# Kernel optimization log

Hardware: AMD Instinct MI355X
Metric: run time of the kernel (lower is better)

The kernel has to match this reference:

```python
import jax, jax.numpy as jnp
import numpy as np

SIZE = 48          # sinkhorn_canvas_size
EPS = 0.01         # entropy regularization
ITERS = 5          # sinkhorn iterations
CHANNEL = 0        # fixed channel (original picks a random one of 3)


def _build_cost_matrix(size):
    y, x = jnp.meshgrid(jnp.arange(size), jnp.arange(size), indexing='ij')
    pixels = jnp.stack((y.flatten(), x.flatten()), axis=1).astype(jnp.float32) / size  # [N,2]
    diff = pixels[:, None, :] - pixels[None, :, :]  # [N,N,2]
    return jnp.sum(diff * diff, axis=-1)            # [N,N]


def setup_inputs() -> dict:
    key = jax.random.key(0)
    k1, k2 = jax.random.split(key)
    B = 32
    img_pred = jax.random.uniform(k1, (B, 3, SIZE, SIZE), dtype=jnp.float32)
    img_target = jax.random.uniform(k2, (B, 3, SIZE, SIZE), dtype=jnp.float32)
    cost_matrix = _build_cost_matrix(SIZE)
    return {"img_pred": img_pred, "img_target": img_target, "cost_matrix": cost_matrix}


def reference(img_pred, img_target, cost_matrix):
    B = img_pred.shape[0]
    # fixed channel, flatten spatial dims -> [B, N]
    p = img_pred[:, CHANNEL].reshape(B, -1) + 1e-9
    t = img_target[:, CHANNEL].reshape(B, -1) + 1e-9
    mass_source = p / jnp.sum(p, axis=-1, keepdims=True)
    mass_target = t / jnp.sum(t, axis=-1, keepdims=True)
    log_u = jnp.log(mass_source)
    log_v = jnp.log(mass_target)
    u = jnp.zeros_like(mass_source)
    v = jnp.zeros_like(mass_target)

    def M(u, v):
        # modified cost for log-domain updates: [B, N, N]
        return (-cost_matrix[None, :, :] + u[:, :, None] + v[:, None, :]) / EPS

    def lse(A):
        # matches torch: log(sum(exp(A), axis=2) + 1e-6)
        return jnp.log(jnp.sum(jnp.exp(A), axis=2) + 1e-6)

    for _ in range(ITERS):
        u = EPS * (log_u - lse(M(u, v))) + u
        v = EPS * (log_v - lse(jnp.swapaxes(M(u, v), 1, 2))) + v

    P = jnp.exp(M(u, v))                               # [B, N, N]
    cost = jnp.sum(P * cost_matrix[None, :, :], axis=(1, 2))  # [B]
    return cost
```

## Files before the change

### kernel.cpp

```cpp
#include <hip/hip_runtime.h>


#define SZ 48
#define SN 2304
#define LD 52
#define NBAT 32
#define NTHR 1024
#define NW 16
#define YB 3

__global__ __launch_bounds__(256) void k_pre(const float* __restrict__ C,
                                             float* __restrict__ G,
                                             float* __restrict__ H) {
    const int idx = blockIdx.x * 256 + threadIdx.x;
    const int a = idx / SZ;
    const int c = idx - a * SZ;
    const float cv = C[(size_t)a * SZ * SN + (size_t)c * SZ];
    const float g = expf(-100.f * cv);
    G[idx] = g;
    H[idx] = g * cv;
}

__device__ __forceinline__ float getc(const float4 v, int i) {
    return i == 0 ? v.x : i == 1 ? v.y : i == 2 ? v.z : v.w;
}

__global__ __launch_bounds__(NTHR) void k_sink(const float* __restrict__ pred,
                                               const float* __restrict__ tgt,
                                               const float* __restrict__ Gm,
                                               const float* __restrict__ Hm,
                                               float* __restrict__ out) {
    __shared__ float Fa[SZ * LD];
    __shared__ float Fb[SZ * LD];
    __shared__ float Fms[SZ * LD];
    __shared__ float Fmt[SZ * LD];
    __shared__ float Tt[SZ * LD];
    __shared__ float gsl[SZ];
    __shared__ float red[32];

    const int t = threadIdx.x;
    const int b = blockIdx.x;
    const int l = t & 63;
    const int w = __builtin_amdgcn_readfirstlane(t >> 6);
    const int r0 = w * YB;

    if (t < SZ) {
        float s = 0.f;
        #pragma unroll 8
        for (int j = 0; j < SZ; ++j) s += Gm[t * SZ + j];
        gsl[t] = s;
    }
    const float* __restrict__ pg = pred + (size_t)b * 3 * SN;
    const float* __restrict__ tg = tgt + (size_t)b * 3 * SN;
    float sp = 0.f, st = 0.f;
    for (int i = t; i < SN; i += NTHR) {
        const float vp = pg[i] + 1e-9f;
        const float vt = tg[i] + 1e-9f;
        const int y = i / SZ, x = i - y * SZ;
        Fms[y * LD + x] = vp;
        Fmt[y * LD + x] = vt;
        sp += vp; st += vt;
    }
    #pragma unroll
    for (int off = 32; off; off >>= 1) {
        sp += __shfl_down(sp, off);
        st += __shfl_down(st, off);
    }
    if (l == 0) { red[w] = sp; red[16 + w] = st; }
    __syncthreads();
    float ps = 0.f, ts = 0.f;
    #pragma unroll
    for (int k = 0; k < NW; ++k) { ps += red[k]; ts += red[16 + k]; }
    for (int i = t; i < SN; i += NTHR) {
        const int y = i / SZ, x = i - y * SZ;
        const float ms = Fms[y * LD + x] / ps;
        Fms[y * LD + x] = ms;
        Fmt[y * LD + x] /= ts;
        Fa[y * LD + x] = ms / (gsl[y] * gsl[x] + 1e-6f);
        Fb[y * LD + x] = 1.f;
    }
    __syncthreads();

    for (int p = 1; p < 10; ++p) {
        float* __restrict__ src = (p & 1) ? Fa : Fb;
        float* __restrict__ dst = (p & 1) ? Fb : Fa;
        const float* __restrict__ mv = (p & 1) ? Fmt : Fms;

        if (l < SZ) {
            float a0 = 0.f, a1 = 0.f, a2 = 0.f;
            #pragma unroll
            for (int jc = 0; jc < 12; ++jc) {
                const float4 q = *(const float4*)&src[l * LD + jc * 4];
                #pragma unroll
                for (int jj = 0; jj < 4; ++jj) {
                    const int j = jc * 4 + jj;
                    const float g0 = Gm[j * SZ + r0];
                    const float g1 = Gm[j * SZ + r0 + 1];
                    const float g2 = Gm[j * SZ + r0 + 2];
                    const float v = getc(q, jj);
                    a0 = fmaf(g0, v, a0);
                    a1 = fmaf(g1, v, a1);
                    a2 = fmaf(g2, v, a2);
                }
            }
            Tt[(r0 + 0) * LD + l] = a0;
            Tt[(r0 + 1) * LD + l] = a1;
            Tt[(r0 + 2) * LD + l] = a2;
        }
        __syncthreads();

        if (l < SZ) {
            float a0 = 0.f, a1 = 0.f, a2 = 0.f;
            #pragma unroll
            for (int jc = 0; jc < 12; ++jc) {
                const float4 q = *(const float4*)&Tt[l * LD + jc * 4];
                #pragma unroll
                for (int jj = 0; jj < 4; ++jj) {
                    const int j = jc * 4 + jj;
                    const float g0 = Gm[j * SZ + r0];
                    const float g1 = Gm[j * SZ + r0 + 1];
                    const float g2 = Gm[j * SZ + r0 + 2];
                    const float v = getc(q, jj);
                    a0 = fmaf(g0, v, a0);
                    a1 = fmaf(g1, v, a1);
                    a2 = fmaf(g2, v, a2);
                }
            }
            const float s3[3] = {a0, a1, a2};
            #pragma unroll
            for (int k = 0; k < YB; ++k) {
                const int idx = (r0 + k) * LD + l;
                const float yo = dst[idx];
                dst[idx] = mv[idx] * yo / (yo * s3[k] + 1e-6f);
            }
        }
        __syncthreads();
    }

    if (l < SZ) {
        float t1[3] = {0.f, 0.f, 0.f}, t2[3] = {0.f, 0.f, 0.f};
        #pragma unroll
        for (int jc = 0; jc < 12; ++jc) {
            const float4 q = *(const float4*)&Fb[l * LD + jc * 4];
            #pragma unroll
            for (int jj = 0; jj < 4; ++jj) {
                const int j = jc * 4 + jj;
                const float v = getc(q, jj);
                #pragma unroll
                for (int k = 0; k < YB; ++k) {
                    t1[k] = fmaf(Gm[j * SZ + r0 + k], v, t1[k]);
                    t2[k] = fmaf(Hm[j * SZ + r0 + k], v, t2[k]);
                }
            }
        }
        #pragma unroll
        for (int k = 0; k < YB; ++k) {
            Tt [(r0 + k) * LD + l] = t1[k];
            Fms[(r0 + k) * LD + l] = t2[k];
        }
    }
    __syncthreads();

    float part = 0.f;
    if (l < SZ) {
        float u[3] = {0.f, 0.f, 0.f};
        #pragma unroll
        for (int jc = 0; jc < 12; ++jc) {
            const float4 q1 = *(const float4*)&Tt [l * LD + jc * 4];
            const float4 q2 = *(const float4*)&Fms[l * LD + jc * 4];
            #pragma unroll
            for (int jj = 0; jj < 4; ++jj) {
                const int j = jc * 4 + jj;
                const float v1 = getc(q1, jj);
                const float v2 = getc(q2, jj);
                #pragma unroll
                for (int k = 0; k < YB; ++k) {
                    u[k] = fmaf(Hm[j * SZ + r0 + k], v1, u[k]);
                    u[k] = fmaf(Gm[j * SZ + r0 + k], v2, u[k]);
                }
            }
        }
        #pragma unroll
        for (int k = 0; k < YB; ++k)
            part = fmaf(Fa[(r0 + k) * LD + l], u[k], part);
    }
    #pragma unroll
    for (int off = 32; off; off >>= 1) part += __shfl_down(part, off);
    if (l == 0) red[w] = part;
    __syncthreads();
    if (t == 0) {
        float c = 0.f;
        #pragma unroll
        for (int k = 0; k < NW; ++k) c += red[k];
        out[b] = c;
    }
}

extern "C" void kernel_launch(void* const* d_in, const int* in_sizes, int n_in,
                              void* d_out, int out_size, void* d_ws, size_t ws_size,
                              hipStream_t stream) {
    const float* pred = (const float*)d_in[0];
    const float* tgt  = (const float*)d_in[1];
    const float* C    = (const float*)d_in[2];
    float* G = (float*)d_ws;
    float* H = G + SN;

    k_pre<<<9, 256, 0, stream>>>(C, G, H);
    k_sink<<<NBAT, NTHR, 0, stream>>>(pred, tgt, G, H, (float*)d_out);
}
```

Measured before the change: 115.7 us.

## Fuse Gaussian kernel precompute into Sinkhorn kernel and stage G/H in LDS

Removes the separate precompute launch and has every batch block build the separable Gaussian factors G and H in shared memory straight from the cost matrix. The matvec loops then read G/H as float4 from LDS rather than scalar global loads. Each wave now handles 4 rows instead of 3, so the block shrinks to 768 threads. This saves one launch and global-memory traffic, at the cost of redundant exp work per block and more LDS use.

```diff
diff --git a/kernel.cpp b/kernel.cpp
--- a/kernel.cpp
+++ b/kernel.cpp
@@ -5,21 +5,9 @@
 #define SN 2304
 #define LD 52
 #define NBAT 32
-#define NTHR 1024
-#define NW 16
-#define YB 3
-
-__global__ __launch_bounds__(256) void k_pre(const float* __restrict__ C,
-                                             float* __restrict__ G,
-                                             float* __restrict__ H) {
-    const int idx = blockIdx.x * 256 + threadIdx.x;
-    const int a = idx / SZ;
-    const int c = idx - a * SZ;
-    const float cv = C[(size_t)a * SZ * SN + (size_t)c * SZ];
-    const float g = expf(-100.f * cv);
-    G[idx] = g;
-    H[idx] = g * cv;
-}
+#define NTHR 768
+#define NW 12
+#define YB 4
 
 __device__ __forceinline__ float getc(const float4 v, int i) {
     return i == 0 ? v.x : i == 1 ? v.y : i == 2 ? v.z : v.w;
@@ -27,14 +15,15 @@
 
 __global__ __launch_bounds__(NTHR) void k_sink(const float* __restrict__ pred,
                                                const float* __restrict__ tgt,
-                                               const float* __restrict__ Gm,
-                                               const float* __restrict__ Hm,
+                                               const float* __restrict__ C,
                                                float* __restrict__ out) {
     __shared__ float Fa[SZ * LD];
     __shared__ float Fb[SZ * LD];
     __shared__ float Fms[SZ * LD];
     __shared__ float Fmt[SZ * LD];
     __shared__ float Tt[SZ * LD];
+    __shared__ float Gs[SZ * SZ];
+    __shared__ float Hs[SZ * SZ];
     __shared__ float gsl[SZ];
     __shared__ float red[32];
 
@@ -44,12 +33,14 @@
     const int w = __builtin_amdgcn_readfirstlane(t >> 6);
     const int r0 = w * YB;
 
-    if (t < SZ) {
-        float s = 0.f;
-        #pragma unroll 8
-        for (int j = 0; j < SZ; ++j) s += Gm[t * SZ + j];
-        gsl[t] = s;
-    }
+    for (int i = t; i < SN; i += NTHR) {
+        const int a = i / SZ, c = i - a * SZ;
+        const float cv = C[(size_t)a * SZ * SN + (size_t)c * SZ];
+        const float g = expf(-100.f * cv);
+        Gs[a * SZ + c] = g;
+        Hs[a * SZ + c] = g * cv;
+    }
+
     const float* __restrict__ pg = pred + (size_t)b * 3 * SN;
     const float* __restrict__ tg = tgt + (size_t)b * 3 * SN;
     float sp = 0.f, st = 0.f;
@@ -68,9 +59,18 @@
     }
     if (l == 0) { red[w] = sp; red[16 + w] = st; }
     __syncthreads();
+
+    if (t < SZ) {
+        float s = 0.f;
+        #pragma unroll 8
+        for (int j = 0; j < SZ; ++j) s += Gs[t * SZ + j];
+        gsl[t] = s;
+    }
     float ps = 0.f, ts = 0.f;
     #pragma unroll
     for (int k = 0; k < NW; ++k) { ps += red[k]; ts += red[16 + k]; }
+    __syncthreads();
+
     for (int i = t; i < SN; i += NTHR) {
         const int y = i / SZ, x = i - y * SZ;
         const float ms = Fms[y * LD + x] / ps;
@@ -87,70 +87,70 @@
         const float* __restrict__ mv = (p & 1) ? Fmt : Fms;
 
         if (l < SZ) {
-            float a0 = 0.f, a1 = 0.f, a2 = 0.f;
+            float a0 = 0.f, a1 = 0.f, a2 = 0.f, a3 = 0.f;
             #pragma unroll
             for (int jc = 0; jc < 12; ++jc) {
                 const float4 q = *(const float4*)&src[l * LD + jc * 4];
                 #pragma unroll
                 for (int jj = 0; jj < 4; ++jj) {
                     const int j = jc * 4 + jj;
-                    const float g0 = Gm[j * SZ + r0];
-                    const float g1 = Gm[j * SZ + r0 + 1];
-                    const float g2 = Gm[j * SZ + r0 + 2];
+                    const float4 g = *(const float4*)&Gs[j * SZ + r0];
                     const float v = getc(q, jj);
-                    a0 = fmaf(g0, v, a0);
-                    a1 = fmaf(g1, v, a1);
-                    a2 = fmaf(g2, v, a2);
+                    a0 = fmaf(g.x, v, a0);
+                    a1 = fmaf(g.y, v, a1);
+                    a2 = fmaf(g.z, v, a2);
+                    a3 = fmaf(g.w, v, a3);
                 }
             }
             Tt[(r0 + 0) * LD + l] = a0;
             Tt[(r0 + 1) * LD + l] = a1;
             Tt[(r0 + 2) * LD + l] = a2;
+            Tt[(r0 + 3) * LD + l] = a3;
         }
         __syncthreads();
 
         if (l < SZ) {
-            float a0 = 0.f, a1 = 0.f, a2 = 0.f;
+            float a0 = 0.f, a1 = 0.f, a2 = 0.f, a3 = 0.f;
             #pragma unroll
             for (int jc = 0; jc < 12; ++jc) {
                 const float4 q = *(const float4*)&Tt[l * LD + jc * 4];
                 #pragma unroll
                 for (int jj = 0; jj < 4; ++jj) {
                     const int j = jc * 4 + jj;
-                    const float g0 = Gm[j * SZ + r0];
-                    const float g1 = Gm[j * SZ + r0 + 1];
-                    const float g2 = Gm[j * SZ + r0 + 2];
+                    const float4 g = *(const float4*)&Gs[j * SZ + r0];
                     const float v = getc(q, jj);
-                    a0 = fmaf(g0, v, a0);
-                    a1 = fmaf(g1, v, a1);
-                    a2 = fmaf(g2, v, a2);
+                    a0 = fmaf(g.x, v, a0);
+                    a1 = fmaf(g.y, v, a1);
+                    a2 = fmaf(g.z, v, a2);
+                    a3 = fmaf(g.w, v, a3);
                 }
             }
-            const float s3[3] = {a0, a1, a2};
+            const float s4[4] = {a0, a1, a2, a3};
             #pragma unroll
             for (int k = 0; k < YB; ++k) {
                 const int idx = (r0 + k) * LD + l;
                 const float yo = dst[idx];
-                dst[idx] = mv[idx] * yo / (yo * s3[k] + 1e-6f);
+                dst[idx] = mv[idx] * yo / (yo * s4[k] + 1e-6f);
             }
         }
         __syncthreads();
     }
 
     if (l < SZ) {
-        float t1[3] = {0.f, 0.f, 0.f}, t2[3] = {0.f, 0.f, 0.f};
+        float t1[4] = {0.f, 0.f, 0.f, 0.f}, t2[4] = {0.f, 0.f, 0.f, 0.f};
         #pragma unroll
         for (int jc = 0; jc < 12; ++jc) {
             const float4 q = *(const float4*)&Fb[l * LD + jc * 4];
             #pragma unroll
             for (int jj = 0; jj < 4; ++jj) {
                 const int j = jc * 4 + jj;
+                const float4 g = *(const float4*)&Gs[j * SZ + r0];
+                const float4 h = *(const float4*)&Hs[j * SZ + r0];
                 const float v = getc(q, jj);
-                #pragma unroll
-                for (int k = 0; k < YB; ++k) {
-                    t1[k] = fmaf(Gm[j * SZ + r0 + k], v, t1[k]);
-                    t2[k] = fmaf(Hm[j * SZ + r0 + k], v, t2[k]);
-                }
+                t1[0] = fmaf(g.x, v, t1[0]);  t1[1] = fmaf(g.y, v, t1[1]);
+                t1[2] = fmaf(g.z, v, t1[2]);  t1[3] = fmaf(g.w, v, t1[3]);
+                t2[0] = fmaf(h.x, v, t2[0]);  t2[1] = fmaf(h.y, v, t2[1]);
+                t2[2] = fmaf(h.z, v, t2[2]);  t2[3] = fmaf(h.w, v, t2[3]);
             }
         }
         #pragma unroll
@@ -163,7 +163,7 @@
 
     float part = 0.f;
     if (l < SZ) {
-        float u[3] = {0.f, 0.f, 0.f};
+        float u[4] = {0.f, 0.f, 0.f, 0.f};
         #pragma unroll
         for (int jc = 0; jc < 12; ++jc) {
             const float4 q1 = *(const float4*)&Tt [l * LD + jc * 4];
@@ -171,13 +171,14 @@
             #pragma unroll
             for (int jj = 0; jj < 4; ++jj) {
                 const int j = jc * 4 + jj;
+                const float4 g = *(const float4*)&Gs[j * SZ + r0];
+                const float4 h = *(const float4*)&Hs[j * SZ + r0];
                 const float v1 = getc(q1, jj);
                 const float v2 = getc(q2, jj);
-                #pragma unroll
-                for (int k = 0; k < YB; ++k) {
-                    u[k] = fmaf(Hm[j * SZ + r0 + k], v1, u[k]);
-                    u[k] = fmaf(Gm[j * SZ + r0 + k], v2, u[k]);
-                }
+                u[0] = fmaf(h.x, v1, u[0]);  u[1] = fmaf(h.y, v1, u[1]);
+                u[2] = fmaf(h.z, v1, u[2]);  u[3] = fmaf(h.w, v1, u[3]);
+                u[0] = fmaf(g.x, v2, u[0]);  u[1] = fmaf(g.y, v2, u[1]);
+                u[2] = fmaf(g.z, v2, u[2]);  u[3] = fmaf(g.w, v2, u[3]);
             }
         }
         #pragma unroll
@@ -202,9 +203,5 @@
     const float* pred = (const float*)d_in[0];
     const float* tgt  = (const float*)d_in[1];
     const float* C    = (const float*)d_in[2];
-    float* G = (float*)d_ws;
-    float* H = G + SN;
-
-    k_pre<<<9, 256, 0, stream>>>(C, G, H);
-    k_sink<<<NBAT, NTHR, 0, stream>>>(pred, tgt, G, H, (float*)d_out);
+    k_sink<<<NBAT, NTHR, 0, stream>>>(pred, tgt, C, (float*)d_out);
 }
```

Measured after the change: 106.6 us. -7.9%, faster.

## Use 12 waves with 4 rows each and keep scaling vectors in registers

Applied to the files above, without the earlier changes.

Reduces the block from 16 to 12 wavefronts, with each wave computing 4 output rows so the separable Gaussian matrix can be read as float4 scalar loads. The dual scaling vectors and marginals are kept in registers rather than reread from shared memory. Shared rows are preloaded into register arrays before the FMA chains, the input load is vectorised to float4, and the padding lanes now compute on clamped indices instead of branching. This cuts global and LDS load instructions and divergence, at the cost of higher register pressure and fewer waves per block.

```diff
diff --git a/kernel.cpp b/kernel.cpp
--- a/kernel.cpp
+++ b/kernel.cpp
@@ -5,9 +5,9 @@
 #define SN 2304
 #define LD 52
 #define NBAT 32
-#define NTHR 1024
-#define NW 16
-#define YB 3
+#define NTHR 768
+#define NW 12
+#define YB 4
 
 __global__ __launch_bounds__(256) void k_pre(const float* __restrict__ C,
                                              float* __restrict__ G,
@@ -25,15 +25,39 @@
     return i == 0 ? v.x : i == 1 ? v.y : i == 2 ? v.z : v.w;
 }
 
-__global__ __launch_bounds__(NTHR) void k_sink(const float* __restrict__ pred,
-                                               const float* __restrict__ tgt,
-                                               const float* __restrict__ Gm,
-                                               const float* __restrict__ Hm,
-                                               float* __restrict__ out) {
-    __shared__ float Fa[SZ * LD];
-    __shared__ float Fb[SZ * LD];
-    __shared__ float Fms[SZ * LD];
-    __shared__ float Fmt[SZ * LD];
+__device__ __forceinline__ void conv4(const float* __restrict__ rowp,
+                                      const float* __restrict__ Mm,
+                                      int r0, float out[4]) {
+    float4 q[12];
+    #pragma unroll
+    for (int jc = 0; jc < 12; ++jc)
+        q[jc] = *(const float4*)&rowp[jc * 4];
+    float a0 = 0.f, a1 = 0.f, a2 = 0.f, a3 = 0.f;
+    #pragma unroll
+    for (int jc = 0; jc < 12; ++jc) {
+        #pragma unroll
+        for (int jj = 0; jj < 4; ++jj) {
+            const int j = jc * 4 + jj;
+            const float4 g = *(const float4*)&Mm[j * SZ + r0];
+            const float v = getc(q[jc], jj);
+            a0 = fmaf(g.x, v, a0);
+            a1 = fmaf(g.y, v, a1);
+            a2 = fmaf(g.z, v, a2);
+            a3 = fmaf(g.w, v, a3);
+        }
+    }
+    out[0] = a0; out[1] = a1; out[2] = a2; out[3] = a3;
+}
+
+__global__ __launch_bounds__(NTHR, 1) void k_sink(const float* __restrict__ pred,
+                                                  const float* __restrict__ tgt,
+                                                  const float* __restrict__ Gm,
+                                                  const float* __restrict__ Hm,
+                                                  float* __restrict__ out) {
+    __shared__ float FaL[SZ * LD];
+    __shared__ float FbL[SZ * LD];
+    __shared__ float FmsL[SZ * LD];
+    __shared__ float FmtL[SZ * LD];
     __shared__ float Tt[SZ * LD];
     __shared__ float gsl[SZ];
     __shared__ float red[32];
@@ -43,6 +67,7 @@
     const int l = t & 63;
     const int w = __builtin_amdgcn_readfirstlane(t >> 6);
     const int r0 = w * YB;
+    const int lc = (l < SZ) ? l : 0;
 
     if (t < SZ) {
         float s = 0.f;
@@ -50,16 +75,20 @@
         for (int j = 0; j < SZ; ++j) s += Gm[t * SZ + j];
         gsl[t] = s;
     }
-    const float* __restrict__ pg = pred + (size_t)b * 3 * SN;
-    const float* __restrict__ tg = tgt + (size_t)b * 3 * SN;
+    const float4* __restrict__ pg4 =
+        (const float4*)(pred + (size_t)b * 3 * SN);
+    const float4* __restrict__ tg4 =
+        (const float4*)(tgt + (size_t)b * 3 * SN);
     float sp = 0.f, st = 0.f;
-    for (int i = t; i < SN; i += NTHR) {
-        const float vp = pg[i] + 1e-9f;
-        const float vt = tg[i] + 1e-9f;
-        const int y = i / SZ, x = i - y * SZ;
-        Fms[y * LD + x] = vp;
-        Fmt[y * LD + x] = vt;
-        sp += vp; st += vt;
+    if (t < 576) {
+        const int y = t / 12, xc = (t - y * 12) * 4;
+        float4 vp = pg4[t], vt = tg4[t];
+        vp.x += 1e-9f; vp.y += 1e-9f; vp.z += 1e-9f; vp.w += 1e-9f;
+        vt.x += 1e-9f; vt.y += 1e-9f; vt.z += 1e-9f; vt.w += 1e-9f;
+        *(float4*)&FmsL[y * LD + xc] = vp;
+        *(float4*)&FmtL[y * LD + xc] = vt;
+        sp = vp.x + vp.y + vp.z + vp.w;
+        st = vt.x + vt.y + vt.z + vt.w;
     }
     #pragma unroll
     for (int off = 32; off; off >>= 1) {
@@ -71,118 +100,117 @@
     float ps = 0.f, ts = 0.f;
     #pragma unroll
     for (int k = 0; k < NW; ++k) { ps += red[k]; ts += red[16 + k]; }
-    for (int i = t; i < SN; i += NTHR) {
-        const int y = i / SZ, x = i - y * SZ;
-        const float ms = Fms[y * LD + x] / ps;
-        Fms[y * LD + x] = ms;
-        Fmt[y * LD + x] /= ts;
-        Fa[y * LD + x] = ms / (gsl[y] * gsl[x] + 1e-6f);
-        Fb[y * LD + x] = 1.f;
-    }
-    __syncthreads();
-
+
+    float ms[4], mt[4], fa[4], fb[4];
+    {
+        const float gx = gsl[lc];
+        #pragma unroll
+        for (int k = 0; k < YB; ++k) {
+            ms[k] = FmsL[(r0 + k) * LD + lc] / ps;
+            mt[k] = FmtL[(r0 + k) * LD + lc] / ts;
+            fa[k] = ms[k] / (gsl[r0 + k] * gx + 1e-6f);
+            fb[k] = 1.f;
+        }
+        if (l < SZ) {
+            #pragma unroll
+            for (int k = 0; k < YB; ++k) {
+                FaL[(r0 + k) * LD + l] = fa[k];
+                FbL[(r0 + k) * LD + l] = 1.f;
+            }
+        }
+    }
+    __syncthreads();
+
+    #pragma unroll 1
     for (int p = 1; p < 10; ++p) {
-        float* __restrict__ src = (p & 1) ? Fa : Fb;
-        float* __restrict__ dst = (p & 1) ? Fb : Fa;
-        const float* __restrict__ mv = (p & 1) ? Fmt : Fms;
-
-        if (l < SZ) {
-            float a0 = 0.f, a1 = 0.f, a2 = 0.f;
-            #pragma unroll
-            for (int jc = 0; jc < 12; ++jc) {
-                const float4 q = *(const float4*)&src[l * LD + jc * 4];
-                #pragma unroll
-                for (int jj = 0; jj < 4; ++jj) {
-                    const int j = jc * 4 + jj;
-                    const float g0 = Gm[j * SZ + r0];
-                    const float g1 = Gm[j * SZ + r0 + 1];
-                    const float g2 = Gm[j * SZ + r0 + 2];
-                    const float v = getc(q, jj);
-                    a0 = fmaf(g0, v, a0);
-                    a1 = fmaf(g1, v, a1);
-                    a2 = fmaf(g2, v, a2);
-                }
-            }
-            Tt[(r0 + 0) * LD + l] = a0;
-            Tt[(r0 + 1) * LD + l] = a1;
-            Tt[(r0 + 2) * LD + l] = a2;
+        const float* __restrict__ srcp = (p & 1) ? FaL : FbL;
+        float* __restrict__ dstp       = (p & 1) ? FbL : FaL;
+        float* dreg                    = (p & 1) ? fb : fa;
+        const float* mvr               = (p & 1) ? mt : ms;
+
+        float s4[4];
+        conv4(&srcp[lc * LD], Gm, r0, s4);
+        if (l < SZ) {
+            Tt[(r0 + 0) * LD + l] = s4[0];
+            Tt[(r0 + 1) * LD + l] = s4[1];
+            Tt[(r0 + 2) * LD + l] = s4[2];
+            Tt[(r0 + 3) * LD + l] = s4[3];
         }
         __syncthreads();
 
-        if (l < SZ) {
-            float a0 = 0.f, a1 = 0.f, a2 = 0.f;
-            #pragma unroll
-            for (int jc = 0; jc < 12; ++jc) {
-                const float4 q = *(const float4*)&Tt[l * LD + jc * 4];
-                #pragma unroll
-                for (int jj = 0; jj < 4; ++jj) {
-                    const int j = jc * 4 + jj;
-                    const float g0 = Gm[j * SZ + r0];
-                    const float g1 = Gm[j * SZ + r0 + 1];
-                    const float g2 = Gm[j * SZ + r0 + 2];
-                    const float v = getc(q, jj);
-                    a0 = fmaf(g0, v, a0);
-                    a1 = fmaf(g1, v, a1);
-                    a2 = fmaf(g2, v, a2);
-                }
-            }
-            const float s3[3] = {a0, a1, a2};
-            #pragma unroll
-            for (int k = 0; k < YB; ++k) {
-                const int idx = (r0 + k) * LD + l;
-                const float yo = dst[idx];
-                dst[idx] = mv[idx] * yo / (yo * s3[k] + 1e-6f);
-            }
+        conv4(&Tt[lc * LD], Gm, r0, s4);
+        #pragma unroll
+        for (int k = 0; k < YB; ++k) {
+            const float yo = dreg[k];
+            dreg[k] = mvr[k] * yo / (yo * s4[k] + 1e-6f);
+        }
+        if (l < SZ) {
+            #pragma unroll
+            for (int k = 0; k < YB; ++k)
+                dstp[(r0 + k) * LD + l] = dreg[k];
         }
         __syncthreads();
     }
 
-    if (l < SZ) {
-        float t1[3] = {0.f, 0.f, 0.f}, t2[3] = {0.f, 0.f, 0.f};
+    {
+        float4 q[12];
+        #pragma unroll
+        for (int jc = 0; jc < 12; ++jc)
+            q[jc] = *(const float4*)&FbL[lc * LD + jc * 4];
+        float t1[4] = {0.f, 0.f, 0.f, 0.f}, t2[4] = {0.f, 0.f, 0.f, 0.f};
         #pragma unroll
         for (int jc = 0; jc < 12; ++jc) {
-            const float4 q = *(const float4*)&Fb[l * LD + jc * 4];
             #pragma unroll
             for (int jj = 0; jj < 4; ++jj) {
                 const int j = jc * 4 + jj;
-                const float v = getc(q, jj);
-                #pragma unroll
-                for (int k = 0; k < YB; ++k) {
-                    t1[k] = fmaf(Gm[j * SZ + r0 + k], v, t1[k]);
-                    t2[k] = fmaf(Hm[j * SZ + r0 + k], v, t2[k]);
-                }
-            }
-        }
-        #pragma unroll
-        for (int k = 0; k < YB; ++k) {
-            Tt [(r0 + k) * LD + l] = t1[k];
-            Fms[(r0 + k) * LD + l] = t2[k];
+                const float4 g = *(const float4*)&Gm[j * SZ + r0];
+                const float4 h = *(const float4*)&Hm[j * SZ + r0];
+                const float v = getc(q[jc], jj);
+                t1[0] = fmaf(g.x, v, t1[0]);  t1[1] = fmaf(g.y, v, t1[1]);
+                t1[2] = fmaf(g.z, v, t1[2]);  t1[3] = fmaf(g.w, v, t1[3]);
+                t2[0] = fmaf(h.x, v, t2[0]);  t2[1] = fmaf(h.y, v, t2[1]);
+                t2[2] = fmaf(h.z, v, t2[2]);  t2[3] = fmaf(h.w, v, t2[3]);
+            }
+        }
+        if (l < SZ) {
+            #pragma unroll
+            for (int k = 0; k < YB; ++k) {
+                Tt  [(r0 + k) * LD + l] = t1[k];
+                FmsL[(r0 + k) * LD + l] = t2[k];
+            }
         }
     }
     __syncthreads();
 
     float part = 0.f;
-    if (l < SZ) {
-        float u[3] = {0.f, 0.f, 0.f};
+    {
+        float4 q1[12], q2[12];
         #pragma unroll
         for (int jc = 0; jc < 12; ++jc) {
-            const float4 q1 = *(const float4*)&Tt [l * LD + jc * 4];
-            const float4 q2 = *(const float4*)&Fms[l * LD + jc * 4];
+            q1[jc] = *(const float4*)&Tt  [lc * LD + jc * 4];
+            q2[jc] = *(const float4*)&FmsL[lc * LD + jc * 4];
+        }
+        float u[4] = {0.f, 0.f, 0.f, 0.f};
+        #pragma unroll
+        for (int jc = 0; jc < 12; ++jc) {
             #pragma unroll
             for (int jj = 0; jj < 4; ++jj) {
                 const int j = jc * 4 + jj;
-                const float v1 = getc(q1, jj);
-                const float v2 = getc(q2, jj);
-                #pragma unroll
-                for (int k = 0; k < YB; ++k) {
-                    u[k] = fmaf(Hm[j * SZ + r0 + k], v1, u[k]);
-                    u[k] = fmaf(Gm[j * SZ + r0 + k], v2, u[k]);
-                }
-            }
-        }
-        #pragma unroll
-        for (int k = 0; k < YB; ++k)
-            part = fmaf(Fa[(r0 + k) * LD + l], u[k], part);
+                const float4 g = *(const float4*)&Gm[j * SZ + r0];
+                const float4 h = *(const float4*)&Hm[j * SZ + r0];
+                const float v1 = getc(q1[jc], jj);
+                const float v2 = getc(q2[jc], jj);
+                u[0] = fmaf(h.x, v1, u[0]);  u[1] = fmaf(h.y, v1, u[1]);
+                u[2] = fmaf(h.z, v1, u[2]);  u[3] = fmaf(h.w, v1, u[3]);
+                u[0] = fmaf(g.x, v2, u[0]);  u[1] = fmaf(g.y, v2, u[1]);
+                u[2] = fmaf(g.z, v2, u[2]);  u[3] = fmaf(g.w, v2, u[3]);
+            }
+        }
+        if (l < SZ) {
+            #pragma unroll
+            for (int k = 0; k < YB; ++k)
+                part = fmaf(fa[k], u[k], part);
+        }
     }
     #pragma unroll
     for (int off = 32; off; off >>= 1) part += __shfl_down(part, off);
```

New measurement: 139.6 us. +20.7%, slower.
